# Performance work log

Measured on AMD Instinct MI355X. Metric: run time of the kernel, lower is better.

The kernel has to match this reference:

```python
import jax, jax.numpy as jnp
import numpy as np
from jax import lax

B, H, W, C = 8, 256, 256, 64
REDUCTION = 8
LENGTH = 9
HIDDEN = max(8, C // REDUCTION)


def _conv(x, w, b, pad='SAME'):
    y = lax.conv_general_dilated(x, w, (1, 1), pad,
                                 dimension_numbers=('NHWC', 'HWIO', 'NHWC'))
    return y + b


def _bilinear_sample(img, y, x):
    # img: [B,H,W,C]; y,x: [B,H,W] float coords
    Bi, Hi, Wi, _ = img.shape
    y0 = jnp.floor(y)
    x0 = jnp.floor(x)
    y0i = jnp.clip(y0.astype(jnp.int32), 0, Hi - 1)
    x0i = jnp.clip(x0.astype(jnp.int32), 0, Wi - 1)
    y1i = jnp.clip((y0 + 1.0).astype(jnp.int32), 0, Hi - 1)
    x1i = jnp.clip((x0 + 1.0).astype(jnp.int32), 0, Wi - 1)
    b = jnp.arange(Bi)[:, None, None]
    Ia = img[b, y0i, x0i]
    Ib = img[b, y1i, x0i]
    Ic = img[b, y0i, x1i]
    Id = img[b, y1i, x1i]
    # weights use CLIPPED integer corner coords (faithful to the TF source)
    y0f = y0i.astype(img.dtype)
    x0f = x0i.astype(img.dtype)
    y1f = y1i.astype(img.dtype)
    x1f = x1i.astype(img.dtype)
    wa = ((x1f - x) * (y1f - y))[..., None]
    wb = ((x1f - x) * (y - y0f))[..., None]
    wc = ((x - x0f) * (y1f - y))[..., None]
    wd = ((x - x0f) * (y - y0f))[..., None]
    return wa * Ia + wb * Ib + wc * Ic + wd * Id


def _oriented_pool(x, vx, vy):
    # x: [B,H,W,C]; vx,vy: [B,H,W] unit direction components
    _, Hi, Wi, _ = x.shape
    yy = jnp.arange(Hi, dtype=x.dtype)[None, :, None]  # broadcasts to [B,H,W]
    xx = jnp.arange(Wi, dtype=x.dtype)[None, None, :]
    half = LENGTH // 2
    acc = jnp.zeros_like(x)
    for t in range(-half, half + 1):  # fixed small set of offsets
        tf_ = jnp.asarray(t, dtype=x.dtype)
        cy = yy + tf_ * vy
        cx = xx + tf_ * vx
        acc = acc + _bilinear_sample(x, cy, cx)
    return acc / jnp.asarray(LENGTH, dtype=x.dtype)


def setup_inputs() -> dict:
    key = jax.random.key(0)
    ks = jax.random.split(key, 9)
    s = 0.05
    return {
        'x': jax.random.normal(ks[0], (B, H, W, C), jnp.float32),
        'w3': jax.random.normal(ks[1], (3, 3, C, HIDDEN), jnp.float32) * s,
        'b3': jnp.zeros((HIDDEN,), jnp.float32),
        'w1': jax.random.normal(ks[2], (1, 1, HIDDEN, 1), jnp.float32) * s,
        'b1': jnp.zeros((1,), jnp.float32),
        'wr': jax.random.normal(ks[3], (1, 1, 2 * C, HIDDEN), jnp.float32) * s,
        'br': jnp.zeros((HIDDEN,), jnp.float32),
        'we': jax.random.normal(ks[4], (1, 1, HIDDEN, 2 * C), jnp.float32) * s,
        'be': jnp.zeros((2 * C,), jnp.float32),
    }


def reference(x, w3, b3, w1, b1, wr, br, we, be):
    h = jax.nn.relu(_conv(x, w3, b3))                    # [B,H,W,hidden]
    theta = np.pi * jax.nn.sigmoid(_conv(h, w1, b1))     # [B,H,W,1]
    cos_t = jnp.cos(theta)[..., 0]                       # [B,H,W]
    sin_t = jnp.sin(theta)[..., 0]
    tan_feat = _oriented_pool(x, cos_t, sin_t)           # tangential direction
    nor_feat = _oriented_pool(x, -sin_t, cos_t)          # normal direction
    context = jnp.concatenate([tan_feat, nor_feat], axis=-1)  # [B,H,W,2C]
    r = jax.nn.relu(_conv(context, wr, br))
    w = jax.nn.sigmoid(_conv(r, we, be))                 # [B,H,W,2C]
    alpha_tan, alpha_norm = jnp.split(w, 2, axis=-1)
    return (alpha_tan + alpha_norm) * x
```

## Files before the change

kernel.cpp:

```cpp
#include <hip/hip_runtime.h>
#include <math.h>

#define Bq 8
#define Hq 256
#define Wq 256
#define Cq 64
#define HID 8
#define PI_F 3.14159265358979323846f

__device__ __forceinline__ float wred(float v) {
    v += __shfl_xor(v, 32, 64);
    v += __shfl_xor(v, 16, 64);
    v += __shfl_xor(v, 8, 64);
    v += __shfl_xor(v, 4, 64);
    v += __shfl_xor(v, 2, 64);
    v += __shfl_xor(v, 1, 64);
    return v;
}

__device__ __forceinline__ float bilin(const float* __restrict__ img,
                                       float cy, float cx, int lane) {
    float fy0 = floorf(cy);
    float fx0 = floorf(cx);
    int y0 = (int)fy0;
    int x0 = (int)fx0;
    int y0i = min(max(y0, 0), Hq - 1);
    int x0i = min(max(x0, 0), Wq - 1);
    int y1i = min(max(y0 + 1, 0), Hq - 1);
    int x1i = min(max(x0 + 1, 0), Wq - 1);
    float y0f = (float)y0i, x0f = (float)x0i;
    float y1f = (float)y1i, x1f = (float)x1i;
    float wy0 = y1f - cy;
    float wy1 = cy - y0f;
    float wx0 = x1f - cx;
    float wx1 = cx - x0f;
    float Ia = img[((size_t)(y0i * Wq) + x0i) * Cq + lane];
    float Ib = img[((size_t)(y1i * Wq) + x0i) * Cq + lane];
    float Ic = img[((size_t)(y0i * Wq) + x1i) * Cq + lane];
    float Id = img[((size_t)(y1i * Wq) + x1i) * Cq + lane];
    return (wx0 * wy0) * Ia + (wx0 * wy1) * Ib + (wx1 * wy0) * Ic + (wx1 * wy1) * Id;
}

__global__ __launch_bounds__(256) void oca_kernel(
    const float* __restrict__ x,
    const float* __restrict__ w3, const float* __restrict__ b3,
    const float* __restrict__ w1, const float* __restrict__ b1,
    const float* __restrict__ wr, const float* __restrict__ br,
    const float* __restrict__ we, const float* __restrict__ be,
    float* __restrict__ out) {
    const int wid  = blockIdx.x * (blockDim.x >> 6) + (threadIdx.x >> 6);
    const int lane = threadIdx.x & 63;
    const int b  = wid >> 16;
    const int yq = (wid >> 8) & 255;
    const int xq = wid & 255;
    const float* img = x + (size_t)b * (Hq * (size_t)Wq * Cq);

    float hacc[HID];
#pragma unroll
    for (int j = 0; j < HID; ++j) hacc[j] = 0.f;
#pragma unroll
    for (int dy = -1; dy <= 1; ++dy) {
        int yy = yq + dy;
        if ((unsigned)yy >= (unsigned)Hq) continue;
#pragma unroll
        for (int dx = -1; dx <= 1; ++dx) {
            int xx = xq + dx;
            if ((unsigned)xx >= (unsigned)Wq) continue;
            float xv = img[((size_t)(yy * Wq) + xx) * Cq + lane];
            const float* wp = w3 + (size_t)(((dy + 1) * 3 + (dx + 1)) * Cq + lane) * HID;
            float4 w0 = *(const float4*)(wp);
            float4 w1v = *(const float4*)(wp + 4);
            hacc[0] = fmaf(xv, w0.x, hacc[0]);
            hacc[1] = fmaf(xv, w0.y, hacc[1]);
            hacc[2] = fmaf(xv, w0.z, hacc[2]);
            hacc[3] = fmaf(xv, w0.w, hacc[3]);
            hacc[4] = fmaf(xv, w1v.x, hacc[4]);
            hacc[5] = fmaf(xv, w1v.y, hacc[5]);
            hacc[6] = fmaf(xv, w1v.z, hacc[6]);
            hacc[7] = fmaf(xv, w1v.w, hacc[7]);
        }
    }
    float h[HID];
#pragma unroll
    for (int j = 0; j < HID; ++j) {
        float s = wred(hacc[j]) + b3[j];
        h[j] = fmaxf(s, 0.f);
    }

    float z = b1[0];
#pragma unroll
    for (int j = 0; j < HID; ++j) z = fmaf(h[j], w1[j], z);
    float theta = PI_F / (1.f + expf(-z));
    float ct = cosf(theta);
    float st = sinf(theta);

    const float fy = (float)yq, fx = (float)xq;
    float acc_t = 0.f, acc_n = 0.f;
#pragma unroll
    for (int t = -4; t <= 4; ++t) {
        float tf = (float)t;
        acc_t += bilin(img, fy + tf * st, fx + tf * ct, lane);
        acc_n += bilin(img, fy + tf * ct, fx - tf * st, lane);
    }
    float tanv = acc_t / 9.0f;
    float norv = acc_n / 9.0f;

    const float* wrp0 = wr + (size_t)lane * HID;
    const float* wrp1 = wr + (size_t)(64 + lane) * HID;
    float4 a0 = *(const float4*)(wrp0);
    float4 a1 = *(const float4*)(wrp0 + 4);
    float4 c0 = *(const float4*)(wrp1);
    float4 c1 = *(const float4*)(wrp1 + 4);
    float p[HID];
    p[0] = fmaf(tanv, a0.x, norv * c0.x);
    p[1] = fmaf(tanv, a0.y, norv * c0.y);
    p[2] = fmaf(tanv, a0.z, norv * c0.z);
    p[3] = fmaf(tanv, a0.w, norv * c0.w);
    p[4] = fmaf(tanv, a1.x, norv * c1.x);
    p[5] = fmaf(tanv, a1.y, norv * c1.y);
    p[6] = fmaf(tanv, a1.z, norv * c1.z);
    p[7] = fmaf(tanv, a1.w, norv * c1.w);
    float r[HID];
#pragma unroll
    for (int j = 0; j < HID; ++j) {
        float s = wred(p[j]) + br[j];
        r[j] = fmaxf(s, 0.f);
    }

    float zt = be[lane];
    float zn = be[64 + lane];
#pragma unroll
    for (int j = 0; j < HID; ++j) {
        zt = fmaf(r[j], we[(size_t)j * 128 + lane], zt);
        zn = fmaf(r[j], we[(size_t)j * 128 + 64 + lane], zn);
    }
    float wt = 1.f / (1.f + expf(-zt));
    float wn = 1.f / (1.f + expf(-zn));
    float xc = img[((size_t)(yq * Wq) + xq) * Cq + lane];
    out[(size_t)wid * Cq + lane] = (wt + wn) * xc;
}

extern "C" void kernel_launch(void* const* d_in, const int* in_sizes, int n_in,
                              void* d_out, int out_size, void* d_ws, size_t ws_size,
                              hipStream_t stream) {
    const float* x  = (const float*)d_in[0];
    const float* w3 = (const float*)d_in[1];
    const float* b3 = (const float*)d_in[2];
    const float* w1 = (const float*)d_in[3];
    const float* b1 = (const float*)d_in[4];
    const float* wr = (const float*)d_in[5];
    const float* br = (const float*)d_in[6];
    const float* we = (const float*)d_in[7];
    const float* be = (const float*)d_in[8];
    float* out = (float*)d_out;

    const int total_waves = Bq * Hq * Wq;
    const int waves_per_block = 4;
    dim3 grid(total_waves / waves_per_block), block(256);
    oca_kernel<<<grid, block, 0, stream>>>(x, w3, b3, w1, b1, wr, br, we, be, out);
}
```

Measured before the change: 1.036 ms.

## Fold 8-way wave reductions, scalarize bilinear indices, use fast math intrinsics

The eight separate 64-lane butterfly reductions are replaced with a transpose-fold that leaves each lane holding one of the eight hidden sums, which cuts the shuffle count from 48 to about 10 per reduction. The per-lane results are then rebroadcast with shuffles for the expand layer. Bilinear corner indices and the wave id are made wave-uniform through readfirstlane, so address arithmetic can run on scalar registers. expf, cosf, sinf and division are swapped for fast intrinsics and rcp, which trades some accuracy for fewer instructions.

```diff
diff --git a/kernel.cpp b/kernel.cpp
--- a/kernel.cpp
+++ b/kernel.cpp
@@ -8,36 +8,51 @@
 #define HID 8
 #define PI_F 3.14159265358979323846f
 
-__device__ __forceinline__ float wred(float v) {
-    v += __shfl_xor(v, 32, 64);
-    v += __shfl_xor(v, 16, 64);
-    v += __shfl_xor(v, 8, 64);
-    v += __shfl_xor(v, 4, 64);
-    v += __shfl_xor(v, 2, 64);
-    v += __shfl_xor(v, 1, 64);
-    return v;
+__device__ __forceinline__ float fold8(float v0, float v1, float v2, float v3,
+                                       float v4, float v5, float v6, float v7,
+                                       int lane) {
+    const bool b4 = (lane & 4) != 0;
+    float k0 = b4 ? v4 : v0, g0 = b4 ? v0 : v4;
+    float k1 = b4 ? v5 : v1, g1 = b4 ? v1 : v5;
+    float k2 = b4 ? v6 : v2, g2 = b4 ? v2 : v6;
+    float k3 = b4 ? v7 : v3, g3 = b4 ? v3 : v7;
+    k0 += __shfl_xor(g0, 4, 64);
+    k1 += __shfl_xor(g1, 4, 64);
+    k2 += __shfl_xor(g2, 4, 64);
+    k3 += __shfl_xor(g3, 4, 64);
+    const bool b2 = (lane & 2) != 0;
+    float m0 = b2 ? k2 : k0, n0 = b2 ? k0 : k2;
+    float m1 = b2 ? k3 : k1, n1 = b2 ? k1 : k3;
+    m0 += __shfl_xor(n0, 2, 64);
+    m1 += __shfl_xor(n1, 2, 64);
+    const bool b1_ = (lane & 1) != 0;
+    float q = b1_ ? m1 : m0, r = b1_ ? m0 : m1;
+    q += __shfl_xor(r, 1, 64);
+    q += __shfl_xor(q, 8, 64);
+    q += __shfl_xor(q, 16, 64);
+    q += __shfl_xor(q, 32, 64);
+    return q;
 }
 
-__device__ __forceinline__ float bilin(const float* __restrict__ img,
-                                       float cy, float cx, int lane) {
+__device__ __forceinline__ float bilin_s(const float* __restrict__ img,
+                                         float cy, float cx, int lane) {
     float fy0 = floorf(cy);
     float fx0 = floorf(cx);
-    int y0 = (int)fy0;
-    int x0 = (int)fx0;
+    int y0 = __builtin_amdgcn_readfirstlane((int)fy0);
+    int x0 = __builtin_amdgcn_readfirstlane((int)fx0);
     int y0i = min(max(y0, 0), Hq - 1);
     int x0i = min(max(x0, 0), Wq - 1);
     int y1i = min(max(y0 + 1, 0), Hq - 1);
     int x1i = min(max(x0 + 1, 0), Wq - 1);
-    float y0f = (float)y0i, x0f = (float)x0i;
-    float y1f = (float)y1i, x1f = (float)x1i;
-    float wy0 = y1f - cy;
-    float wy1 = cy - y0f;
-    float wx0 = x1f - cx;
-    float wx1 = cx - x0f;
-    float Ia = img[((size_t)(y0i * Wq) + x0i) * Cq + lane];
-    float Ib = img[((size_t)(y1i * Wq) + x0i) * Cq + lane];
-    float Ic = img[((size_t)(y0i * Wq) + x1i) * Cq + lane];
-    float Id = img[((size_t)(y1i * Wq) + x1i) * Cq + lane];
+    float wy0 = (float)y1i - cy;
+    float wy1 = cy - (float)y0i;
+    float wx0 = (float)x1i - cx;
+    float wx1 = cx - (float)x0i;
+    const float* pa = img + (size_t)(((y0i << 8) + x0i) << 6);
+    const float* pb = img + (size_t)(((y1i << 8) + x0i) << 6);
+    const float* pc = img + (size_t)(((y0i << 8) + x1i) << 6);
+    const float* pd = img + (size_t)(((y1i << 8) + x1i) << 6);
+    float Ia = pa[lane], Ib = pb[lane], Ic = pc[lane], Id = pd[lane];
     return (wx0 * wy0) * Ia + (wx0 * wy1) * Ib + (wx1 * wy0) * Ic + (wx1 * wy1) * Id;
 }
 
@@ -48,16 +63,15 @@
     const float* __restrict__ wr, const float* __restrict__ br,
     const float* __restrict__ we, const float* __restrict__ be,
     float* __restrict__ out) {
-    const int wid  = blockIdx.x * (blockDim.x >> 6) + (threadIdx.x >> 6);
     const int lane = threadIdx.x & 63;
+    const int wid = __builtin_amdgcn_readfirstlane(blockIdx.x * 4 + (threadIdx.x >> 6));
     const int b  = wid >> 16;
     const int yq = (wid >> 8) & 255;
     const int xq = wid & 255;
-    const float* img = x + (size_t)b * (Hq * (size_t)Wq * Cq);
+    const float* img = x + ((size_t)b << 22);
 
-    float hacc[HID];
-#pragma unroll
-    for (int j = 0; j < HID; ++j) hacc[j] = 0.f;
+    float h0 = 0.f, h1 = 0.f, h2 = 0.f, h3 = 0.f;
+    float h4 = 0.f, h5 = 0.f, h6 = 0.f, h7 = 0.f;
 #pragma unroll
     for (int dy = -1; dy <= 1; ++dy) {
         int yy = yq + dy;
@@ -66,44 +80,43 @@
         for (int dx = -1; dx <= 1; ++dx) {
             int xx = xq + dx;
             if ((unsigned)xx >= (unsigned)Wq) continue;
-            float xv = img[((size_t)(yy * Wq) + xx) * Cq + lane];
-            const float* wp = w3 + (size_t)(((dy + 1) * 3 + (dx + 1)) * Cq + lane) * HID;
-            float4 w0 = *(const float4*)(wp);
-            float4 w1v = *(const float4*)(wp + 4);
-            hacc[0] = fmaf(xv, w0.x, hacc[0]);
-            hacc[1] = fmaf(xv, w0.y, hacc[1]);
-            hacc[2] = fmaf(xv, w0.z, hacc[2]);
-            hacc[3] = fmaf(xv, w0.w, hacc[3]);
-            hacc[4] = fmaf(xv, w1v.x, hacc[4]);
-            hacc[5] = fmaf(xv, w1v.y, hacc[5]);
-            hacc[6] = fmaf(xv, w1v.z, hacc[6]);
-            hacc[7] = fmaf(xv, w1v.w, hacc[7]);
+            float xv = img[(size_t)(((yy << 8) + xx) << 6) + lane];
+            const float* wp = w3 + (size_t)((((dy + 1) * 3 + dx + 1) << 6) + lane) * HID;
+            float4 wv0 = *(const float4*)(wp);
+            float4 wv1 = *(const float4*)(wp + 4);
+            h0 = fmaf(xv, wv0.x, h0);
+            h1 = fmaf(xv, wv0.y, h1);
+            h2 = fmaf(xv, wv0.z, h2);
+            h3 = fmaf(xv, wv0.w, h3);
+            h4 = fmaf(xv, wv1.x, h4);
+            h5 = fmaf(xv, wv1.y, h5);
+            h6 = fmaf(xv, wv1.z, h6);
+            h7 = fmaf(xv, wv1.w, h7);
         }
     }
-    float h[HID];
-#pragma unroll
-    for (int j = 0; j < HID; ++j) {
-        float s = wred(hacc[j]) + b3[j];
-        h[j] = fmaxf(s, 0.f);
-    }
+    const int j = lane & 7;
+    float hsum = fold8(h0, h1, h2, h3, h4, h5, h6, h7, lane);
+    float h_l = fmaxf(hsum + b3[j], 0.f);
 
-    float z = b1[0];
-#pragma unroll
-    for (int j = 0; j < HID; ++j) z = fmaf(h[j], w1[j], z);
-    float theta = PI_F / (1.f + expf(-z));
-    float ct = cosf(theta);
-    float st = sinf(theta);
+    float zp = h_l * w1[j];
+    zp += __shfl_xor(zp, 1, 64);
+    zp += __shfl_xor(zp, 2, 64);
+    zp += __shfl_xor(zp, 4, 64);
+    float z = zp + b1[0];
+    float theta = PI_F * __builtin_amdgcn_rcpf(1.f + __expf(-z));
+    float ct = __cosf(theta);
+    float st = __sinf(theta);
 
     const float fy = (float)yq, fx = (float)xq;
     float acc_t = 0.f, acc_n = 0.f;
 #pragma unroll
     for (int t = -4; t <= 4; ++t) {
         float tf = (float)t;
-        acc_t += bilin(img, fy + tf * st, fx + tf * ct, lane);
-        acc_n += bilin(img, fy + tf * ct, fx - tf * st, lane);
+        acc_t += bilin_s(img, fmaf(tf, st, fy), fmaf(tf, ct, fx), lane);
+        acc_n += bilin_s(img, fmaf(tf, ct, fy), fmaf(-tf, st, fx), lane);
     }
-    float tanv = acc_t / 9.0f;
-    float norv = acc_n / 9.0f;
+    float tanv = acc_t * (1.f / 9.f);
+    float norv = acc_n * (1.f / 9.f);
 
     const float* wrp0 = wr + (size_t)lane * HID;
     const float* wrp1 = wr + (size_t)(64 + lane) * HID;
@@ -111,33 +124,49 @@
     float4 a1 = *(const float4*)(wrp0 + 4);
     float4 c0 = *(const float4*)(wrp1);
     float4 c1 = *(const float4*)(wrp1 + 4);
-    float p[HID];
-    p[0] = fmaf(tanv, a0.x, norv * c0.x);
-    p[1] = fmaf(tanv, a0.y, norv * c0.y);
-    p[2] = fmaf(tanv, a0.z, norv * c0.z);
-    p[3] = fmaf(tanv, a0.w, norv * c0.w);
-    p[4] = fmaf(tanv, a1.x, norv * c1.x);
-    p[5] = fmaf(tanv, a1.y, norv * c1.y);
-    p[6] = fmaf(tanv, a1.z, norv * c1.z);
-    p[7] = fmaf(tanv, a1.w, norv * c1.w);
-    float r[HID];
-#pragma unroll
-    for (int j = 0; j < HID; ++j) {
-        float s = wred(p[j]) + br[j];
-        r[j] = fmaxf(s, 0.f);
-    }
+    float p0 = fmaf(tanv, a0.x, norv * c0.x);
+    float p1 = fmaf(tanv, a0.y, norv * c0.y);
+    float p2 = fmaf(tanv, a0.z, norv * c0.z);
+    float p3 = fmaf(tanv, a0.w, norv * c0.w);
+    float p4 = fmaf(tanv, a1.x, norv * c1.x);
+    float p5 = fmaf(tanv, a1.y, norv * c1.y);
+    float p6 = fmaf(tanv, a1.z, norv * c1.z);
+    float p7 = fmaf(tanv, a1.w, norv * c1.w);
+    float rsum = fold8(p0, p1, p2, p3, p4, p5, p6, p7, lane);
+    float r_l = fmaxf(rsum + br[j], 0.f);
 
+    float rb0 = r_l;
+    float rb1 = __shfl_xor(rb0, 1, 64);
+    float rb2 = __shfl_xor(rb0, 2, 64);
+    float rb3 = __shfl_xor(rb1, 2, 64);
+    float rb4 = __shfl_xor(rb0, 4, 64);
+    float rb5 = __shfl_xor(rb1, 4, 64);
+    float rb6 = __shfl_xor(rb2, 4, 64);
+    float rb7 = __shfl_xor(rb3, 4, 64);
+
+    const float* web = we + ((size_t)j << 7) + lane;
     float zt = be[lane];
     float zn = be[64 + lane];
-#pragma unroll
-    for (int j = 0; j < HID; ++j) {
-        zt = fmaf(r[j], we[(size_t)j * 128 + lane], zt);
-        zn = fmaf(r[j], we[(size_t)j * 128 + 64 + lane], zn);
-    }
-    float wt = 1.f / (1.f + expf(-zt));
-    float wn = 1.f / (1.f + expf(-zn));
-    float xc = img[((size_t)(yq * Wq) + xq) * Cq + lane];
-    out[(size_t)wid * Cq + lane] = (wt + wn) * xc;
+    zt = fmaf(rb0, web[0],            zt); zn = fmaf(rb0, web[64],            zn);
+    zt = fmaf(rb1, *(const float*)((uintptr_t)web ^ (1u << 9)),        zt);
+    zn = fmaf(rb1, *(const float*)(((uintptr_t)web ^ (1u << 9)) + 256), zn);
+    zt = fmaf(rb2, *(const float*)((uintptr_t)web ^ (2u << 9)),        zt);
+    zn = fmaf(rb2, *(const float*)(((uintptr_t)web ^ (2u << 9)) + 256), zn);
+    zt = fmaf(rb3, *(const float*)((uintptr_t)web ^ (3u << 9)),        zt);
+    zn = fmaf(rb3, *(const float*)(((uintptr_t)web ^ (3u << 9)) + 256), zn);
+    zt = fmaf(rb4, *(const float*)((uintptr_t)web ^ (4u << 9)),        zt);
+    zn = fmaf(rb4, *(const float*)(((uintptr_t)web ^ (4u << 9)) + 256), zn);
+    zt = fmaf(rb5, *(const float*)((uintptr_t)web ^ (5u << 9)),        zt);
+    zn = fmaf(rb5, *(const float*)(((uintptr_t)web ^ (5u << 9)) + 256), zn);
+    zt = fmaf(rb6, *(const float*)((uintptr_t)web ^ (6u << 9)),        zt);
+    zn = fmaf(rb6, *(const float*)(((uintptr_t)web ^ (6u << 9)) + 256), zn);
+    zt = fmaf(rb7, *(const float*)((uintptr_t)web ^ (7u << 9)),        zt);
+    zn = fmaf(rb7, *(const float*)(((uintptr_t)web ^ (7u << 9)) + 256), zn);
+
+    float wt = __builtin_amdgcn_rcpf(1.f + __expf(-zt));
+    float wn = __builtin_amdgcn_rcpf(1.f + __expf(-zn));
+    float xc = img[(size_t)(((yq << 8) + xq) << 6) + lane];
+    out[((size_t)wid << 6) + lane] = (wt + wn) * xc;
 }
 
 extern "C" void kernel_launch(void* const* d_in, const int* in_sizes, int n_in,
@@ -155,7 +184,6 @@
     float* out = (float*)d_out;
 
     const int total_waves = Bq * Hq * Wq;
-    const int waves_per_block = 4;
-    dim3 grid(total_waves / waves_per_block), block(256);
+    dim3 grid(total_waves / 4), block(256);
     oca_kernel<<<grid, block, 0, stream>>>(x, w3, b3, w1, b1, wr, br, we, be, out);
 }
```

Result: faster. 913.8 us (-11.8%).
